# Kernel optimization log

Measured on AMD Instinct MI355X. Metric: run time of the kernel, lower is better.

## Reference

```python
import math
import jax, jax.numpy as jnp
import numpy as np

N_HEADS = 8
D_MODEL = 512
HEAD_DIM = D_MODEL // N_HEADS
N, S = 4, 2048


def setup_inputs() -> dict:
    key = jax.random.key(0)
    ks = jax.random.split(key, 9)
    inp = {
        "value": jax.random.normal(ks[0], (N, S, D_MODEL), dtype=jnp.float32),
        "key": jax.random.normal(ks[1], (N, S, D_MODEL), dtype=jnp.float32),
        "query": jax.random.normal(ks[2], (N, S, D_MODEL), dtype=jnp.float32),
        "mask": jax.random.randint(ks[3], (N, 1, 1, S), 0, 2, dtype=jnp.int32),
        # nn.Linear weights: [out, in]; projections are head_dim x head_dim, shared across heads
        "Wv": jax.random.normal(ks[4], (HEAD_DIM, HEAD_DIM), dtype=jnp.float32) / math.sqrt(HEAD_DIM),
        "Wk": jax.random.normal(ks[5], (HEAD_DIM, HEAD_DIM), dtype=jnp.float32) / math.sqrt(HEAD_DIM),
        "Wq": jax.random.normal(ks[6], (HEAD_DIM, HEAD_DIM), dtype=jnp.float32) / math.sqrt(HEAD_DIM),
        "Wfc": jax.random.normal(ks[7], (D_MODEL, D_MODEL), dtype=jnp.float32) / math.sqrt(D_MODEL),
        "bfc": jax.random.normal(ks[8], (D_MODEL,), dtype=jnp.float32) * 0.01,
    }
    return inp


def reference(value, key, query, mask, Wv, Wk, Wq, Wfc, bfc):
    n = query.shape[0]
    sv, sk, sq = value.shape[1], key.shape[1], query.shape[1]
    # split heads: [N, S, H, D]
    v = value.reshape(n, sv, N_HEADS, HEAD_DIM) @ Wv.T
    k = key.reshape(n, sk, N_HEADS, HEAD_DIM) @ Wk.T
    q = query.reshape(n, sq, N_HEADS, HEAD_DIM) @ Wq.T
    # [N, H, Q, K] scores
    scores = jnp.einsum('nqhd,nkhd->nhqk', q, k)
    scores = jnp.where(mask == 0, jnp.float32(-1e20), scores)
    # NOTE: original divides by sqrt(head_dim) AFTER the masked_fill; kept faithful
    attn = jax.nn.softmax(scores / math.sqrt(HEAD_DIM), axis=3)
    out = jnp.einsum('nhqk,nkhd->nqhd', attn, v).reshape(n, sq, D_MODEL)
    return out @ Wfc.T + bfc
```

## Files before the change

kernel.cpp:

```cpp
#include <hip/hip_runtime.h>
#include <hip/hip_bf16.h>

#define N_B 4
#define SEQ 2048
#define NH 8
#define HD 64
#define DM 512

typedef __attribute__((ext_vector_type(8))) short bf16x8;
typedef __attribute__((ext_vector_type(4))) short bf16x4;
typedef __attribute__((ext_vector_type(4))) float f32x4;

#if __has_builtin(__builtin_amdgcn_exp2f)
#define EXP2(x) __builtin_amdgcn_exp2f(x)
#else
#define EXP2(x) exp2f(x)
#endif

__device__ __forceinline__ unsigned short b16(float f) {
  return __bfloat16_as_ushort(__float2bfloat16(f));
}
__device__ __forceinline__ f32x4 mfma32(bf16x8 a, bf16x8 b, f32x4 c) {
  return __builtin_amdgcn_mfma_f32_16x16x32_bf16(a, b, c, 0, 0, 0);
}
__device__ __forceinline__ f32x4 mfma16k(bf16x4 a, bf16x4 b, f32x4 c) {
  return __builtin_amdgcn_mfma_f32_16x16x16bf16_1k(a, b, c, 0, 0, 0);
}
__device__ __forceinline__ bf16x8 cvt8(const float* p) {
  float4 x = *(const float4*)p;
  float4 y = *(const float4*)(p + 4);
  union { unsigned short s[8]; bf16x8 v; } r;
  r.s[0] = b16(x.x); r.s[1] = b16(x.y); r.s[2] = b16(x.z); r.s[3] = b16(x.w);
  r.s[4] = b16(y.x); r.s[5] = b16(y.y); r.s[6] = b16(y.z); r.s[7] = b16(y.w);
  return r.v;
}
__device__ __forceinline__ bf16x8 cvt8v(float4 x, float4 y) {
  union { unsigned short s[8]; bf16x8 v; } r;
  r.s[0] = b16(x.x); r.s[1] = b16(x.y); r.s[2] = b16(x.z); r.s[3] = b16(x.w);
  r.s[4] = b16(y.x); r.s[5] = b16(y.y); r.s[6] = b16(y.z); r.s[7] = b16(y.w);
  return r.v;
}

__global__ __launch_bounds__(256, 4) void proj_kernel(
    const float* __restrict__ qin, const float* __restrict__ kin, const float* __restrict__ vin,
    const float* __restrict__ Wq, const float* __restrict__ Wk, const float* __restrict__ Wv,
    unsigned short* __restrict__ Qp, unsigned short* __restrict__ Kp, unsigned short* __restrict__ Vp)
{
  __shared__ __align__(16) unsigned short Wl[64][72];
  const int tid = threadIdx.x, lane = tid & 63, w = tid >> 6;
  const int hi = lane >> 4, lo = lane & 15;
  const int z = blockIdx.z, nh = blockIdx.y, n = nh >> 3, h = nh & 7;
  const float* W = z == 0 ? Wq : (z == 1 ? Wk : Wv);
  const int srow = tid >> 2, scol = (tid & 3) * 16;
  *(bf16x8*)&Wl[srow][scol]     = cvt8(&W[srow * 64 + scol]);
  *(bf16x8*)&Wl[srow][scol + 8] = cvt8(&W[srow * 64 + scol + 8]);
  __syncthreads();

  const float* in = z == 0 ? qin : (z == 1 ? kin : vin);
  const int sx = blockIdx.x * 64 + w * 16 + lo;
  const float* src = in + ((size_t)(n * SEQ + sx)) * DM + h * HD + hi * 8;
  bf16x8 a0 = cvt8(src), a1 = cvt8(src + 32);

  f32x4 acc[4];
  #pragma unroll
  for (int t = 0; t < 4; ++t) acc[t] = (f32x4){0.f, 0.f, 0.f, 0.f};
  #pragma unroll
  for (int t = 0; t < 4; ++t) {
    bf16x8 wf0 = *(const bf16x8*)&Wl[t * 16 + lo][hi * 8];
    bf16x8 wf1 = *(const bf16x8*)&Wl[t * 16 + lo][32 + hi * 8];
    acc[t] = mfma32(a0, wf0, acc[t]);
    acc[t] = mfma32(a1, wf1, acc[t]);
  }

  if (z < 2) {
    unsigned short* outp = z == 0 ? Qp : Kp;
    const size_t rowb = (size_t)(nh * SEQ + blockIdx.x * 64 + w * 16 + hi * 4);
    #pragma unroll
    for (int t = 0; t < 4; ++t)
      #pragma unroll
      for (int j = 0; j < 4; ++j)
        outp[(rowb + j) * HD + t * 16 + lo] = b16(acc[t][j]);
  } else {
    const int cb = blockIdx.x * 64 + hi * 16 + w * 4;
    #pragma unroll
    for (int t = 0; t < 4; ++t) {
      union { unsigned short s[4]; uint2 u; } p;
      p.s[0] = b16(acc[t][0]); p.s[1] = b16(acc[t][1]);
      p.s[2] = b16(acc[t][2]); p.s[3] = b16(acc[t][3]);
      *(uint2*)&Vp[((size_t)(nh * HD + t * 16 + lo)) * SEQ + cb] = p.u;
    }
  }
}

__global__ __launch_bounds__(256, 2) void attn_kernel(
    const unsigned short* __restrict__ Qp, const unsigned short* __restrict__ Kp,
    const unsigned short* __restrict__ Vp, const int* __restrict__ mask,
    unsigned short* __restrict__ AO)
{
  __shared__ __align__(16) unsigned short Kl[64][72];
  __shared__ __align__(16) unsigned short Vt[64][72];
  __shared__ float maskf[64];

  const int tid = threadIdx.x, lane = tid & 63, w = tid >> 6;
  const int hi = lane >> 4, lo = lane & 15;
  const int nh = blockIdx.y, n = nh >> 3, h = nh & 7;
  const int qb = blockIdx.x * 128 + w * 32;
  const float CS = 0.18033688011112042f;
  const float THR = 44.0f;

  bf16x8 qa[2][2];
  #pragma unroll
  for (int qs = 0; qs < 2; ++qs) {
    const unsigned short* qsrc = Qp + ((size_t)(nh * SEQ + qb + qs * 16 + lo)) * HD + hi * 8;
    qa[qs][0] = *(const bf16x8*)qsrc;
    qa[qs][1] = *(const bf16x8*)(qsrc + 32);
  }

  f32x4 o[2][4];
  #pragma unroll
  for (int qs = 0; qs < 2; ++qs)
    #pragma unroll
    for (int dt = 0; dt < 4; ++dt) o[qs][dt] = (f32x4){0.f, 0.f, 0.f, 0.f};
  float m[2] = {-1e30f, -1e30f}, l[2] = {0.f, 0.f};

  const int srow = tid >> 2, scol = (tid & 3) * 16;
  const unsigned short* Kb = Kp + ((size_t)(nh * SEQ + srow)) * HD + scol;
  const unsigned short* Vb = Vp + ((size_t)(nh * HD + srow)) * SEQ + scol;
  const int* Mb = mask + n * SEQ;

  int4 kr0 = *(const int4*)Kb, kr1 = *(const int4*)(Kb + 8);
  int4 vr0 = *(const int4*)Vb, vr1 = *(const int4*)(Vb + 8);
  int mp = (tid < 64) ? Mb[tid] : 0;

  for (int kv = 0; kv < SEQ / 64; ++kv) {
    __syncthreads();
    *(int4*)&Kl[srow][scol] = kr0; *(int4*)&Kl[srow][scol + 8] = kr1;
    *(int4*)&Vt[srow][scol] = vr0; *(int4*)&Vt[srow][scol + 8] = vr1;
    if (tid < 64) maskf[tid] = mp ? 1.f : 0.f;
    {
      const int kb2 = ((kv + 1) & 31) * 64;
      kr0 = *(const int4*)(Kb + (size_t)kb2 * HD);
      kr1 = *(const int4*)(Kb + (size_t)kb2 * HD + 8);
      vr0 = *(const int4*)(Vb + kb2);
      vr1 = *(const int4*)(Vb + kb2 + 8);
      if (tid < 64) mp = Mb[kb2 + tid];
    }
    __syncthreads();

    bf16x8 ka[4][2];
    #pragma unroll
    for (int t = 0; t < 4; ++t) {
      ka[t][0] = *(const bf16x8*)&Kl[t * 16 + lo][hi * 8];
      ka[t][1] = *(const bf16x8*)&Kl[t * 16 + lo][32 + hi * 8];
    }
    union V16 { bf16x8 v8[2]; bf16x4 v4[4]; };
    V16 vv[4];
    #pragma unroll
    for (int dt = 0; dt < 4; ++dt) {
      vv[dt].v8[0] = *(const bf16x8*)&Vt[dt * 16 + lo][hi * 16];
      vv[dt].v8[1] = *(const bf16x8*)&Vt[dt * 16 + lo][hi * 16 + 8];
    }
    f32x4 mb[4];
    #pragma unroll
    for (int t = 0; t < 4; ++t) mb[t] = *(const f32x4*)&maskf[t * 16 + hi * 4];

    #pragma unroll
    for (int qs = 0; qs < 2; ++qs) {
      f32x4 st[4];
      #pragma unroll
      for (int t = 0; t < 4; ++t) {
        st[t] = mfma32(ka[t][0], qa[qs][0], (f32x4){0.f, 0.f, 0.f, 0.f});
        st[t] = mfma32(ka[t][1], qa[qs][1], st[t]);
      }
      f32x4 mx;
      #pragma unroll
      for (int j = 0; j < 4; ++j)
        mx[j] = fmaxf(fmaxf(st[0][j], st[1][j]), fmaxf(st[2][j], st[3][j]));
      float mxx = fmaxf(fmaxf(mx[0], mx[1]), fmaxf(mx[2], mx[3]));
      mxx = fmaxf(mxx, __shfl_xor(mxx, 16));
      mxx = fmaxf(mxx, __shfl_xor(mxx, 32));
      if (!__all(mxx - m[qs] <= THR)) {
        const float nm = fmaxf(m[qs], mxx);
        const float sc = EXP2((m[qs] - nm) * CS);
        m[qs] = nm;
        l[qs] *= sc;
        #pragma unroll
        for (int dt = 0; dt < 4; ++dt) o[qs][dt] *= sc;
      }
      const float mc = -m[qs] * CS;

      f32x4 pv[4];
      #pragma unroll
      for (int t = 0; t < 4; ++t)
        #pragma unroll
        for (int j = 0; j < 4; ++j)
          pv[t][j] = EXP2(fmaf(st[t][j], CS, mc)) * mb[t][j];
      f32x4 ps = pv[0] + pv[1] + pv[2] + pv[3];
      float prs = ps[0] + ps[1] + ps[2] + ps[3];
      prs += __shfl_xor(prs, 16);
      prs += __shfl_xor(prs, 32);
      l[qs] += prs;

      bf16x4 pf[4];
      #pragma unroll
      for (int t = 0; t < 4; ++t) {
        union { unsigned short s[4]; bf16x4 v; } pu;
        pu.s[0] = b16(pv[t][0]); pu.s[1] = b16(pv[t][1]);
        pu.s[2] = b16(pv[t][2]); pu.s[3] = b16(pv[t][3]);
        pf[t] = pu.v;
      }
      #pragma unroll
      for (int dt = 0; dt < 4; ++dt)
        #pragma unroll
        for (int t = 0; t < 4; ++t)
          o[qs][dt] = mfma16k(vv[dt].v4[t], pf[t], o[qs][dt]);
    }
  }

  #pragma unroll
  for (int qs = 0; qs < 2; ++qs) {
    const float rl = 1.f / l[qs];
    unsigned short* dst = AO + ((size_t)(n * SEQ + qb + qs * 16 + lo)) * DM + h * HD + hi * 4;
    #pragma unroll
    for (int dt = 0; dt < 4; ++dt) {
      f32x4 v = o[qs][dt] * rl;
      union { unsigned short s[4]; uint2 u; } p;
      p.s[0] = b16(v[0]); p.s[1] = b16(v[1]); p.s[2] = b16(v[2]); p.s[3] = b16(v[3]);
      *(uint2*)(dst + dt * 16) = p.u;
    }
  }
}

__global__ __launch_bounds__(256, 4) void fc_kernel(
    const unsigned short* __restrict__ AO, const float* __restrict__ Wfc,
    const float* __restrict__ bfc, float* __restrict__ out)
{
  __shared__ __align__(16) unsigned short Al[64][72];
  __shared__ __align__(16) unsigned short Bl[64][72];
  const int tid = threadIdx.x, lane = tid & 63, w = tid >> 6;
  const int hi = lane >> 4, lo = lane & 15;
  const int rb = blockIdx.x * 64, cb = blockIdx.y * 64;
  const int srow = tid >> 2, scol = (tid & 3) * 16;
  const unsigned short* Ab = AO + (size_t)(rb + srow) * DM + scol;
  const float* Bb = Wfc + (size_t)(cb + srow) * DM + scol;

  int4 ar0 = *(const int4*)Ab, ar1 = *(const int4*)(Ab + 8);
  float4 wr0 = *(const float4*)Bb,        wr1 = *(const float4*)(Bb + 4);
  float4 wr2 = *(const float4*)(Bb + 8),  wr3 = *(const float4*)(Bb + 12);

  f32x4 acc[4];
  #pragma unroll
  for (int t = 0; t < 4; ++t) acc[t] = (f32x4){0.f, 0.f, 0.f, 0.f};

  for (int i = 0; i < 8; ++i) {
    __syncthreads();
    *(int4*)&Al[srow][scol] = ar0; *(int4*)&Al[srow][scol + 8] = ar1;
    *(bf16x8*)&Bl[srow][scol]     = cvt8v(wr0, wr1);
    *(bf16x8*)&Bl[srow][scol + 8] = cvt8v(wr2, wr3);
    {
      const int kn = ((i + 1) & 7) * 64;
      ar0 = *(const int4*)(Ab + kn); ar1 = *(const int4*)(Ab + kn + 8);
      wr0 = *(const float4*)(Bb + kn);      wr1 = *(const float4*)(Bb + kn + 4);
      wr2 = *(const float4*)(Bb + kn + 8);  wr3 = *(const float4*)(Bb + kn + 12);
    }
    __syncthreads();

    bf16x8 a0 = *(const bf16x8*)&Al[w * 16 + lo][hi * 8];
    bf16x8 a1 = *(const bf16x8*)&Al[w * 16 + lo][32 + hi * 8];
    #pragma unroll
    for (int t = 0; t < 4; ++t) {
      bf16x8 w0 = *(const bf16x8*)&Bl[t * 16 + lo][hi * 8];
      bf16x8 w1 = *(const bf16x8*)&Bl[t * 16 + lo][32 + hi * 8];
      acc[t] = mfma32(a0, w0, acc[t]);
      acc[t] = mfma32(a1, w1, acc[t]);
    }
  }

  const int rowb = rb + w * 16 + hi * 4;
  #pragma unroll
  for (int t = 0; t < 4; ++t) {
    const float bias = bfc[cb + t * 16 + lo];
    #pragma unroll
    for (int j = 0; j < 4; ++j)
      out[(size_t)(rowb + j) * DM + cb + t * 16 + lo] = acc[t][j] + bias;
  }
}

extern "C" void kernel_launch(void* const* d_in, const int* in_sizes, int n_in,
                              void* d_out, int out_size, void* d_ws, size_t ws_size,
                              hipStream_t stream) {
  const float* value = (const float*)d_in[0];
  const float* key   = (const float*)d_in[1];
  const float* query = (const float*)d_in[2];
  const int*   mask  = (const int*)d_in[3];
  const float* Wv    = (const float*)d_in[4];
  const float* Wk    = (const float*)d_in[5];
  const float* Wq    = (const float*)d_in[6];
  const float* Wfc   = (const float*)d_in[7];
  const float* bfc   = (const float*)d_in[8];
  float* out = (float*)d_out;

  const size_t per = (size_t)N_B * NH * SEQ * HD;
  unsigned short* Qp = (unsigned short*)d_ws;
  unsigned short* Kp = Qp + per;
  unsigned short* Vp = Kp + per;
  unsigned short* AO = Vp + per;

  proj_kernel<<<dim3(SEQ / 64, N_B * NH, 3), 256, 0, stream>>>(
      query, key, value, Wq, Wk, Wv, Qp, Kp, Vp);
  attn_kernel<<<dim3(SEQ / 128, N_B * NH), 256, 0, stream>>>(Qp, Kp, Vp, mask, AO);
  fc_kernel<<<dim3(N_B * SEQ / 64, DM / 64), 256, 0, stream>>>(AO, Wfc, bfc, out);
}
```

Baseline: 197.0 us.

## Double-buffer LDS tiles in attention and FC kernels, vectorize Q/K projection stores

The attention and FC kernels now keep two LDS buffers and write the next tile into the spare buffer after computing on the current one. This removes one of the two __syncthreads per iteration and lets global loads overlap with compute. The Q/K projection swaps the MFMA operand order so each lane holds contiguous output columns, allowing packed 8-byte stores instead of scattered 2-byte stores. The cost is double the LDS footprint, which may reduce occupancy in the attention kernel.

New measurement: 191.8 us. -2.6%, faster.

```diff
diff --git a/kernel.cpp b/kernel.cpp
--- a/kernel.cpp
+++ b/kernel.cpp
@@ -64,23 +64,34 @@
   f32x4 acc[4];
   #pragma unroll
   for (int t = 0; t < 4; ++t) acc[t] = (f32x4){0.f, 0.f, 0.f, 0.f};
+  bf16x8 wf0[4], wf1[4];
   #pragma unroll
   for (int t = 0; t < 4; ++t) {
-    bf16x8 wf0 = *(const bf16x8*)&Wl[t * 16 + lo][hi * 8];
-    bf16x8 wf1 = *(const bf16x8*)&Wl[t * 16 + lo][32 + hi * 8];
-    acc[t] = mfma32(a0, wf0, acc[t]);
-    acc[t] = mfma32(a1, wf1, acc[t]);
+    wf0[t] = *(const bf16x8*)&Wl[t * 16 + lo][hi * 8];
+    wf1[t] = *(const bf16x8*)&Wl[t * 16 + lo][32 + hi * 8];
   }
 
   if (z < 2) {
+    #pragma unroll
+    for (int t = 0; t < 4; ++t) {
+      acc[t] = mfma32(wf0[t], a0, acc[t]);
+      acc[t] = mfma32(wf1[t], a1, acc[t]);
+    }
     unsigned short* outp = z == 0 ? Qp : Kp;
-    const size_t rowb = (size_t)(nh * SEQ + blockIdx.x * 64 + w * 16 + hi * 4);
-    #pragma unroll
-    for (int t = 0; t < 4; ++t)
-      #pragma unroll
-      for (int j = 0; j < 4; ++j)
-        outp[(rowb + j) * HD + t * 16 + lo] = b16(acc[t][j]);
+    unsigned short* dst = outp + ((size_t)(nh * SEQ + sx)) * HD + hi * 4;
+    #pragma unroll
+    for (int t = 0; t < 4; ++t) {
+      union { unsigned short s[4]; uint2 u; } p;
+      p.s[0] = b16(acc[t][0]); p.s[1] = b16(acc[t][1]);
+      p.s[2] = b16(acc[t][2]); p.s[3] = b16(acc[t][3]);
+      *(uint2*)(dst + t * 16) = p.u;
+    }
   } else {
+    #pragma unroll
+    for (int t = 0; t < 4; ++t) {
+      acc[t] = mfma32(a0, wf0[t], acc[t]);
+      acc[t] = mfma32(a1, wf1[t], acc[t]);
+    }
     const int cb = blockIdx.x * 64 + hi * 16 + w * 4;
     #pragma unroll
     for (int t = 0; t < 4; ++t) {
@@ -97,9 +108,9 @@
     const unsigned short* __restrict__ Vp, const int* __restrict__ mask,
     unsigned short* __restrict__ AO)
 {
-  __shared__ __align__(16) unsigned short Kl[64][72];
-  __shared__ __align__(16) unsigned short Vt[64][72];
-  __shared__ float maskf[64];
+  __shared__ __align__(16) unsigned short Kl[2][64][72];
+  __shared__ __align__(16) unsigned short Vt[2][64][72];
+  __shared__ float maskf[2][64];
 
   const int tid = threadIdx.x, lane = tid & 63, w = tid >> 6;
   const int hi = lane >> 4, lo = lane & 15;
@@ -128,41 +139,40 @@
   const unsigned short* Vb = Vp + ((size_t)(nh * HD + srow)) * SEQ + scol;
   const int* Mb = mask + n * SEQ;
 
-  int4 kr0 = *(const int4*)Kb, kr1 = *(const int4*)(Kb + 8);
-  int4 vr0 = *(const int4*)Vb, vr1 = *(const int4*)(Vb + 8);
-  int mp = (tid < 64) ? Mb[tid] : 0;
+  {
+    int4 k0 = *(const int4*)Kb, k1 = *(const int4*)(Kb + 8);
+    int4 v0 = *(const int4*)Vb, v1 = *(const int4*)(Vb + 8);
+    *(int4*)&Kl[0][srow][scol] = k0; *(int4*)&Kl[0][srow][scol + 8] = k1;
+    *(int4*)&Vt[0][srow][scol] = v0; *(int4*)&Vt[0][srow][scol + 8] = v1;
+    if (tid < 64) maskf[0][tid] = Mb[tid] ? 1.f : 0.f;
+  }
+  __syncthreads();
 
   for (int kv = 0; kv < SEQ / 64; ++kv) {
-    __syncthreads();
-    *(int4*)&Kl[srow][scol] = kr0; *(int4*)&Kl[srow][scol + 8] = kr1;
-    *(int4*)&Vt[srow][scol] = vr0; *(int4*)&Vt[srow][scol + 8] = vr1;
-    if (tid < 64) maskf[tid] = mp ? 1.f : 0.f;
-    {
-      const int kb2 = ((kv + 1) & 31) * 64;
-      kr0 = *(const int4*)(Kb + (size_t)kb2 * HD);
-      kr1 = *(const int4*)(Kb + (size_t)kb2 * HD + 8);
-      vr0 = *(const int4*)(Vb + kb2);
-      vr1 = *(const int4*)(Vb + kb2 + 8);
-      if (tid < 64) mp = Mb[kb2 + tid];
-    }
-    __syncthreads();
+    const int cur = kv & 1;
+    const int kb2 = ((kv + 1) & 31) * 64;
+    int4 kr0 = *(const int4*)(Kb + (size_t)kb2 * HD);
+    int4 kr1 = *(const int4*)(Kb + (size_t)kb2 * HD + 8);
+    int4 vr0 = *(const int4*)(Vb + kb2);
+    int4 vr1 = *(const int4*)(Vb + kb2 + 8);
+    int mp = (tid < 64) ? Mb[kb2 + tid] : 0;
 
     bf16x8 ka[4][2];
     #pragma unroll
     for (int t = 0; t < 4; ++t) {
-      ka[t][0] = *(const bf16x8*)&Kl[t * 16 + lo][hi * 8];
-      ka[t][1] = *(const bf16x8*)&Kl[t * 16 + lo][32 + hi * 8];
+      ka[t][0] = *(const bf16x8*)&Kl[cur][t * 16 + lo][hi * 8];
+      ka[t][1] = *(const bf16x8*)&Kl[cur][t * 16 + lo][32 + hi * 8];
     }
     union V16 { bf16x8 v8[2]; bf16x4 v4[4]; };
     V16 vv[4];
     #pragma unroll
     for (int dt = 0; dt < 4; ++dt) {
-      vv[dt].v8[0] = *(const bf16x8*)&Vt[dt * 16 + lo][hi * 16];
-      vv[dt].v8[1] = *(const bf16x8*)&Vt[dt * 16 + lo][hi * 16 + 8];
+      vv[dt].v8[0] = *(const bf16x8*)&Vt[cur][dt * 16 + lo][hi * 16];
+      vv[dt].v8[1] = *(const bf16x8*)&Vt[cur][dt * 16 + lo][hi * 16 + 8];
     }
     f32x4 mb[4];
     #pragma unroll
-    for (int t = 0; t < 4; ++t) mb[t] = *(const f32x4*)&maskf[t * 16 + hi * 4];
+    for (int t = 0; t < 4; ++t) mb[t] = *(const f32x4*)&maskf[cur][t * 16 + hi * 4];
 
     #pragma unroll
     for (int qs = 0; qs < 2; ++qs) {
@@ -215,6 +225,12 @@
         for (int t = 0; t < 4; ++t)
           o[qs][dt] = mfma16k(vv[dt].v4[t], pf[t], o[qs][dt]);
     }
+
+    const int nxt = cur ^ 1;
+    *(int4*)&Kl[nxt][srow][scol] = kr0; *(int4*)&Kl[nxt][srow][scol + 8] = kr1;
+    *(int4*)&Vt[nxt][srow][scol] = vr0; *(int4*)&Vt[nxt][srow][scol + 8] = vr1;
+    if (tid < 64) maskf[nxt][tid] = mp ? 1.f : 0.f;
+    __syncthreads();
   }
 
   #pragma unroll
@@ -235,8 +251,8 @@
     const unsigned short* __restrict__ AO, const float* __restrict__ Wfc,
     const float* __restrict__ bfc, float* __restrict__ out)
 {
-  __shared__ __align__(16) unsigned short Al[64][72];
-  __shared__ __align__(16) unsigned short Bl[64][72];
+  __shared__ __align__(16) unsigned short Al[2][64][72];
+  __shared__ __align__(16) unsigned short Bl[2][64][72];
   const int tid = threadIdx.x, lane = tid & 63, w = tid >> 6;
   const int hi = lane >> 4, lo = lane & 15;
   const int rb = blockIdx.x * 64, cb = blockIdx.y * 64;
@@ -244,36 +260,42 @@
   const unsigned short* Ab = AO + (size_t)(rb + srow) * DM + scol;
   const float* Bb = Wfc + (size_t)(cb + srow) * DM + scol;
 
-  int4 ar0 = *(const int4*)Ab, ar1 = *(const int4*)(Ab + 8);
-  float4 wr0 = *(const float4*)Bb,        wr1 = *(const float4*)(Bb + 4);
-  float4 wr2 = *(const float4*)(Bb + 8),  wr3 = *(const float4*)(Bb + 12);
+  {
+    int4 a0 = *(const int4*)Ab, a1 = *(const int4*)(Ab + 8);
+    float4 w0 = *(const float4*)Bb,       w1 = *(const float4*)(Bb + 4);
+    float4 w2 = *(const float4*)(Bb + 8), w3 = *(const float4*)(Bb + 12);
+    *(int4*)&Al[0][srow][scol] = a0; *(int4*)&Al[0][srow][scol + 8] = a1;
+    *(bf16x8*)&Bl[0][srow][scol]     = cvt8v(w0, w1);
+    *(bf16x8*)&Bl[0][srow][scol + 8] = cvt8v(w2, w3);
+  }
+  __syncthreads();
 
   f32x4 acc[4];
   #pragma unroll
   for (int t = 0; t < 4; ++t) acc[t] = (f32x4){0.f, 0.f, 0.f, 0.f};
 
   for (int i = 0; i < 8; ++i) {
-    __syncthreads();
-    *(int4*)&Al[srow][scol] = ar0; *(int4*)&Al[srow][scol + 8] = ar1;
-    *(bf16x8*)&Bl[srow][scol]     = cvt8v(wr0, wr1);
-    *(bf16x8*)&Bl[srow][scol + 8] = cvt8v(wr2, wr3);
-    {
-      const int kn = ((i + 1) & 7) * 64;
-      ar0 = *(const int4*)(Ab + kn); ar1 = *(const int4*)(Ab + kn + 8);
-      wr0 = *(const float4*)(Bb + kn);      wr1 = *(const float4*)(Bb + kn + 4);
-      wr2 = *(const float4*)(Bb + kn + 8);  wr3 = *(const float4*)(Bb + kn + 12);
-    }
-    __syncthreads();
-
-    bf16x8 a0 = *(const bf16x8*)&Al[w * 16 + lo][hi * 8];
-    bf16x8 a1 = *(const bf16x8*)&Al[w * 16 + lo][32 + hi * 8];
-    #pragma unroll
-    for (int t = 0; t < 4; ++t) {
-      bf16x8 w0 = *(const bf16x8*)&Bl[t * 16 + lo][hi * 8];
-      bf16x8 w1 = *(const bf16x8*)&Bl[t * 16 + lo][32 + hi * 8];
+    const int cur = i & 1;
+    const int kn = ((i + 1) & 7) * 64;
+    int4 ar0 = *(const int4*)(Ab + kn), ar1 = *(const int4*)(Ab + kn + 8);
+    float4 wr0 = *(const float4*)(Bb + kn),      wr1 = *(const float4*)(Bb + kn + 4);
+    float4 wr2 = *(const float4*)(Bb + kn + 8),  wr3 = *(const float4*)(Bb + kn + 12);
+
+    bf16x8 a0 = *(const bf16x8*)&Al[cur][w * 16 + lo][hi * 8];
+    bf16x8 a1 = *(const bf16x8*)&Al[cur][w * 16 + lo][32 + hi * 8];
+    #pragma unroll
+    for (int t = 0; t < 4; ++t) {
+      bf16x8 w0 = *(const bf16x8*)&Bl[cur][t * 16 + lo][hi * 8];
+      bf16x8 w1 = *(const bf16x8*)&Bl[cur][t * 16 + lo][32 + hi * 8];
       acc[t] = mfma32(a0, w0, acc[t]);
       acc[t] = mfma32(a1, w1, acc[t]);
     }
+
+    const int nxt = cur ^ 1;
+    *(int4*)&Al[nxt][srow][scol] = ar0; *(int4*)&Al[nxt][srow][scol + 8] = ar1;
+    *(bf16x8*)&Bl[nxt][srow][scol]     = cvt8v(wr0, wr1);
+    *(bf16x8*)&Bl[nxt][srow][scol + 8] = cvt8v(wr2, wr3);
+    __syncthreads();
   }
 
   const int rowb = rb + w * 16 + hi * 4;
```
